# Kernel optimization log

Measured on AMD Instinct MI355X. Metric: run time of the kernel, lower is better.

Reference implementation:

```python
import jax, jax.numpy as jnp
import numpy as np

B, T, E = 2, 2048, 2048
H, HKV, DH = 16, 8, 128
G = H // HKV
WINDOW = 512
ROPE_THETA = 10000.0
EPS = 1e-6


def _rms_norm(x, w):
    # Gemma3RMSNorm: fp32 rms_norm with weight = 1 + w
    xf = x.astype(jnp.float32)
    y = xf * jax.lax.rsqrt(jnp.mean(xf * xf, axis=-1, keepdims=True) + EPS)
    return (y * (1.0 + w.astype(jnp.float32))).astype(x.dtype)


def _rotate_half(x):
    x1, x2 = x[..., : DH // 2], x[..., DH // 2 :]
    return jnp.concatenate((-x2, x1), axis=-1)


def setup_inputs() -> dict:
    key = jax.random.key(0)
    ks = jax.random.split(key, 5)
    s = 0.02
    return {
        "x": jax.random.normal(ks[0], (B, T, E), jnp.float32),
        "wq": jax.random.normal(ks[1], (H * DH, E), jnp.float32) * s,
        "wk": jax.random.normal(ks[2], (HKV * DH, E), jnp.float32) * s,
        "wv": jax.random.normal(ks[3], (HKV * DH, E), jnp.float32) * s,
        "wo": jax.random.normal(ks[4], (E, H * DH), jnp.float32) * s,
        "q_norm_w": jnp.zeros((DH,), jnp.float32),
        "k_norm_w": jnp.zeros((DH,), jnp.float32),
    }


def reference(x, wq, wk, wv, wo, q_norm_w, k_norm_w):
    # projections: [B,T,H,DH] -> [B,H,T,DH]
    q = (x @ wq.T).reshape(B, T, H, DH).transpose(0, 2, 1, 3)
    k = (x @ wk.T).reshape(B, T, HKV, DH).transpose(0, 2, 1, 3)
    v = (x @ wv.T).reshape(B, T, HKV, DH).transpose(0, 2, 1, 3)

    # QK-RMSNorm over head_dim
    q = _rms_norm(q, q_norm_w)
    k = _rms_norm(k, k_norm_w)

    # RoPE (prefill: positions 0..T-1)
    pos = jnp.arange(T, dtype=jnp.float32)
    inv_freq = 1.0 / (ROPE_THETA ** (jnp.arange(0, DH, 2, dtype=jnp.float32) / DH))
    freqs = pos[:, None] * inv_freq[None, :]          # [T, DH//2]
    emb = jnp.concatenate((freqs, freqs), axis=-1)    # [T, DH]
    cos = jnp.cos(emb)[None, None, :, :]
    sin = jnp.sin(emb)[None, None, :, :]
    q = q * cos + _rotate_half(q) * sin
    k = k * cos + _rotate_half(k) * sin

    # GQA attention with causal + sliding-window mask, fp32 scores
    q = q * (DH ** -0.5)
    qg = q.reshape(B, HKV, G, T, DH)
    att = jnp.einsum("bhgtd,bhkd->bhgtk", qg.astype(jnp.float32), k.astype(jnp.float32))

    dist = jnp.arange(T)[:, None] - jnp.arange(T)[None, :]   # [T, T]
    mask = (dist >= 0) & (dist <= WINDOW)
    att = jnp.where(mask[None, None, None, :, :], att, jnp.finfo(jnp.float32).min)
    att = jax.nn.softmax(att, axis=-1).astype(q.dtype)

    ctx = jnp.einsum("bhgtk,bhkd->bhgtd", att, v)
    out = ctx.reshape(B, H, T, DH).transpose(0, 2, 1, 3).reshape(B, T, H * DH)
    return out @ wo.T
```

## Files before the change

kernel.cpp:

```cpp
#include <hip/hip_runtime.h>
#include <hip/hip_bf16.h>
#include <stdint.h>

#define B_ 2
#define T_ 2048
#define E_ 2048
#define H_ 16
#define HKV_ 8
#define DH_ 128
#define WINDOW_ 512

typedef unsigned short ush;
typedef float f32x4 __attribute__((ext_vector_type(4)));
typedef __bf16 bf16x8 __attribute__((ext_vector_type(8)));
typedef uint32_t u32x4 __attribute__((ext_vector_type(4)));

static __device__ __forceinline__ ush f2bf(float f) {
    uint32_t u = __float_as_uint(f);
    uint32_t r = (u + 0x7fffu + ((u >> 16) & 1u)) >> 16;
    return (ush)r;
}
static __device__ __forceinline__ float bf2f(ush h) {
    return __uint_as_float(((uint32_t)h) << 16);
}

__global__ __launch_bounds__(256) void cast_kernel(const float* __restrict__ in,
                                                   ush* __restrict__ out, int n4) {
    int i = blockIdx.x * blockDim.x + threadIdx.x;
    if (i >= n4) return;
    float4 f = reinterpret_cast<const float4*>(in)[i];
    ushort4 o;
    o.x = f2bf(f.x); o.y = f2bf(f.y); o.z = f2bf(f.z); o.w = f2bf(f.w);
    reinterpret_cast<ushort4*>(out)[i] = o;
}

template <int MODE>
__global__ __launch_bounds__(256, 2) void gemm_bt(
    const ush* __restrict__ A, const ush* __restrict__ Bm,
    float* __restrict__ Cf, ush* __restrict__ q, ush* __restrict__ k, ush* __restrict__ vT,
    int M, int N, int K)
{
    __shared__ ush As[128 * 64];
    __shared__ ush Bs[128 * 64];
    const int tid = threadIdx.x;
    const int lane = tid & 63;
    const int wid = tid >> 6;
    const int wr = wid >> 1, wc = wid & 1;
    const int gm0 = blockIdx.x * 128, gn0 = blockIdx.y * 128;

    f32x4 acc[4][4] = {};

    const int l8 = lane >> 3;
    const int ce = (lane & 7) * 8;

    for (int kt = 0; kt < K; kt += 64) {
#pragma unroll
        for (int i = 0; i < 4; ++i) {
            const int rowbase = (i * 4 + wid) * 8;
            const int ra = rowbase + l8;
            const ush* ga = A + (size_t)(gm0 + ra) * K + kt + ce;
            __builtin_amdgcn_global_load_lds(
                (const __attribute__((address_space(1))) void*)ga,
                (__attribute__((address_space(3))) void*)(As + rowbase * 64), 16, 0, 0);
            const ush* gb = Bm + (size_t)(gn0 + ra) * K + kt + ce;
            __builtin_amdgcn_global_load_lds(
                (const __attribute__((address_space(1))) void*)gb,
                (__attribute__((address_space(3))) void*)(Bs + rowbase * 64), 16, 0, 0);
        }
        __syncthreads();

#pragma unroll
        for (int s = 0; s < 2; ++s) {
            bf16x8 aF[4], bF[4];
#pragma unroll
            for (int mm = 0; mm < 4; ++mm) {
                int r = wr * 64 + mm * 16 + (lane & 15);
                aF[mm] = *reinterpret_cast<const bf16x8*>(As + r * 64 + s * 32 + ((lane >> 4) * 8));
            }
#pragma unroll
            for (int nn = 0; nn < 4; ++nn) {
                int r = wc * 64 + nn * 16 + (lane & 15);
                bF[nn] = *reinterpret_cast<const bf16x8*>(Bs + r * 64 + s * 32 + ((lane >> 4) * 8));
            }
#pragma unroll
            for (int mm = 0; mm < 4; ++mm)
#pragma unroll
                for (int nn = 0; nn < 4; ++nn)
                    acc[mm][nn] = __builtin_amdgcn_mfma_f32_16x16x32_bf16(
                        aF[mm], bF[nn], acc[mm][nn], 0, 0, 0);
        }
        __syncthreads();
    }

    const int rsub = (lane >> 4) << 2;
    const int csub = lane & 15;
#pragma unroll
    for (int mm = 0; mm < 4; ++mm) {
        const int row0 = gm0 + wr * 64 + mm * 16 + rsub;
#pragma unroll
        for (int nn = 0; nn < 4; ++nn) {
            const int col = gn0 + wc * 64 + nn * 16 + csub;
#pragma unroll
            for (int r = 0; r < 4; ++r) {
                const int row = row0 + r;
                if (MODE == 1) {
                    Cf[(size_t)row * N + col] = acc[mm][nn][r];
                } else {
                    const int bb = row >> 11, tt = row & (T_ - 1);
                    const ush val = f2bf(acc[mm][nn][r]);
                    if (col < H_ * DH_) {
                        const int hh = col >> 7, d = col & 127;
                        q[((((size_t)bb * H_ + hh) * T_ + tt) << 7) + d] = val;
                    } else if (col < H_ * DH_ + HKV_ * DH_) {
                        const int c2 = col - H_ * DH_;
                        const int hh = c2 >> 7, d = c2 & 127;
                        k[((((size_t)bb * HKV_ + hh) * T_ + tt) << 7) + d] = val;
                    } else {
                        const int c2 = col - H_ * DH_ - HKV_ * DH_;
                        const int hh = c2 >> 7, d = c2 & 127;
                        vT[((size_t)((bb * HKV_ + hh) * DH_ + d) << 11) + tt] = val;
                    }
                }
            }
        }
    }
}

__global__ __launch_bounds__(256) void norm_rope(ush* __restrict__ q, ush* __restrict__ k,
                                                 const float* __restrict__ qw,
                                                 const float* __restrict__ kw)
{
    const int lane = threadIdx.x & 63;
    const int row = blockIdx.x * 4 + (threadIdx.x >> 6);
    const int NQ = B_ * H_ * T_;
    ush* p; const float* w; int t; bool isq = (row < NQ);
    if (isq) { p = q + ((size_t)row << 7); t = row & (T_ - 1); w = qw; }
    else     { int r2 = row - NQ; p = k + ((size_t)r2 << 7); t = r2 & (T_ - 1); w = kw; }

    float x0 = bf2f(p[lane]);
    float x1 = bf2f(p[lane + 64]);
    float ss = x0 * x0 + x1 * x1;
#pragma unroll
    for (int off = 32; off; off >>= 1) ss += __shfl_xor(ss, off);
    const float rms = rsqrtf(ss * (1.0f / 128.0f) + 1e-6f);
    float y0 = x0 * rms * (1.0f + w[lane]);
    float y1 = x1 * rms * (1.0f + w[lane + 64]);

    const float invf = expf(-(float)lane * 0.14391156831212787f);
    const float fr = (float)t * invf;
    const float c = cosf(fr), s = sinf(fr);
    float o0 = y0 * c - y1 * s;
    float o1 = y1 * c + y0 * s;
    if (isq) { o0 *= 0.08838834764831845f; o1 *= 0.08838834764831845f; }
    p[lane] = f2bf(o0);
    p[lane + 64] = f2bf(o1);
}

__global__ __launch_bounds__(256) void attn_mfma(const ush* __restrict__ q,
        const ush* __restrict__ k, const ush* __restrict__ vT, ush* __restrict__ ctx)
{
    __shared__ ush Ks[2][32 * 128];
    __shared__ ush Vs[2][128 * 32];
    const int tid = threadIdx.x;
    const int lane = tid & 63;
    const int w = tid >> 6;
    const int g = lane >> 4;
    const int t = lane & 15;

    int bi = blockIdx.x;
    bi = (bi & 7) * 128 + (bi >> 3);
    const int qtile = bi & 31;
    const int hh = (bi >> 5) & 15;
    const int b = bi >> 9;
    const int qb = qtile * 64;
    const int hkv = hh >> 1;

    const ush* qptr = q + ((((size_t)b * H_ + hh) * T_ + qb) << 7);
    const ush* kbase = k + (((size_t)b * HKV_ + hkv) << 18);
    const ush* vtbase = vT + (((size_t)b * HKV_ + hkv) << 18);

    bf16x8 qf[4];
#pragma unroll
    for (int c = 0; c < 4; ++c)
        qf[c] = *reinterpret_cast<const bf16x8*>(qptr + ((16 * w + t) << 7) + 32 * c + 8 * g);

    const int kstart = (qb >= WINDOW_) ? (qb - WINDOW_) : 0;
    const int nt = (qb + 64 - kstart) >> 5;

    auto stage = [&](int ti, int buf) {
        const int kt0 = kstart + (ti << 5);
#pragma unroll
        for (int i = 0; i < 2; ++i) {
            const int C = w * 128 + i * 64 + lane;
            {
                const int row = C >> 4, ch = C & 15;
                const ush* gk = kbase + ((size_t)(kt0 + row) << 7) + ch * 8;
                __builtin_amdgcn_global_load_lds(
                    (const __attribute__((address_space(1))) void*)gk,
                    (__attribute__((address_space(3))) void*)(&Ks[buf][(w * 128 + i * 64) * 8]),
                    16, 0, 0);
            }
            {
                const int row = C >> 2, ch = C & 3;
                const ush* gv = vtbase + ((size_t)row << 11) + kt0 + ch * 8;
                __builtin_amdgcn_global_load_lds(
                    (const __attribute__((address_space(1))) void*)gv,
                    (__attribute__((address_space(3))) void*)(&Vs[buf][(w * 128 + i * 64) * 8]),
                    16, 0, 0);
            }
        }
    };

    float m = -1e30f, lsum = 0.f;
    f32x4 o[8] = {};

    stage(0, 0);
    __syncthreads();

    for (int ti = 0; ti < nt; ++ti) {
        const int cur = ti & 1;
        if (ti + 1 < nt) stage(ti + 1, cur ^ 1);
        const int kt0 = kstart + (ti << 5);
        const int qw0 = qb + 16 * w;
        const bool active = (kt0 + 31 >= qw0 - WINDOW_) && (kt0 <= qw0 + 15);
        if (active) {
            f32x4 st[2] = {};
#pragma unroll
            for (int s = 0; s < 2; ++s)
#pragma unroll
                for (int c = 0; c < 4; ++c) {
                    bf16x8 kf = *reinterpret_cast<const bf16x8*>(
                        &Ks[cur][(16 * s + t) * 128 + 32 * c + 8 * g]);
                    st[s] = __builtin_amdgcn_mfma_f32_16x16x32_bf16(kf, qf[c], st[s], 0, 0, 0);
                }
            const int tg = qb + 16 * w + t;
            float e[2][4];
            float mymax = -3e38f;
#pragma unroll
            for (int s = 0; s < 2; ++s)
#pragma unroll
                for (int r = 0; r < 4; ++r) {
                    const int key = kt0 + 16 * s + 4 * g + r;
                    const int dist = tg - key;
                    const bool valid = (dist >= 0) && (dist <= WINDOW_);
                    const float sv = valid ? st[s][r] : -3e38f;
                    e[s][r] = sv;
                    mymax = fmaxf(mymax, sv);
                }
            mymax = fmaxf(mymax, __shfl_xor(mymax, 16));
            mymax = fmaxf(mymax, __shfl_xor(mymax, 32));
            const float mn = fmaxf(m, mymax);
            const float sc = __expf(m - mn);
            float esum = 0.f;
#pragma unroll
            for (int s = 0; s < 2; ++s)
#pragma unroll
                for (int r = 0; r < 4; ++r) {
                    const float ev = __expf(e[s][r] - mn);
                    e[s][r] = ev;
                    esum += ev;
                }
            esum += __shfl_xor(esum, 16);
            esum += __shfl_xor(esum, 32);
            lsum = lsum * sc + esum;
            m = mn;
#pragma unroll
            for (int ds = 0; ds < 8; ++ds) {
                o[ds][0] *= sc; o[ds][1] *= sc; o[ds][2] *= sc; o[ds][3] *= sc;
            }
            uint32_t word[2][2];
#pragma unroll
            for (int s = 0; s < 2; ++s)
#pragma unroll
                for (int wd = 0; wd < 2; ++wd)
                    word[s][wd] = (uint32_t)f2bf(e[s][2 * wd])
                                | ((uint32_t)f2bf(e[s][2 * wd + 1]) << 16);
            u32x4 bw;
#pragma unroll
            for (int e2 = 0; e2 < 4; ++e2) {
                const int srcl = 16 * (2 * (g & 1) + (e2 >> 1)) + t;
                const uint32_t v0 = __shfl(word[0][e2 & 1], srcl);
                const uint32_t v1 = __shfl(word[1][e2 & 1], srcl);
                bw[e2] = (g >= 2) ? v1 : v0;
            }
            const bf16x8 pF = __builtin_bit_cast(bf16x8, bw);
#pragma unroll
            for (int ds = 0; ds < 8; ++ds) {
                bf16x8 vtF = *reinterpret_cast<const bf16x8*>(
                    &Vs[cur][(16 * ds + t) * 32 + 8 * g]);
                o[ds] = __builtin_amdgcn_mfma_f32_16x16x32_bf16(vtF, pF, o[ds], 0, 0, 0);
            }
        }
        __syncthreads();
    }

    const float linv = 1.0f / lsum;
    ush* cptr = ctx + (((size_t)b * T_ + qb + 16 * w + t) * (H_ * DH_)) + hh * DH_;
#pragma unroll
    for (int ds = 0; ds < 8; ++ds) {
        ushort4 pk;
        pk.x = f2bf(o[ds][0] * linv);
        pk.y = f2bf(o[ds][1] * linv);
        pk.z = f2bf(o[ds][2] * linv);
        pk.w = f2bf(o[ds][3] * linv);
        *reinterpret_cast<ushort4*>(cptr + 16 * ds + 4 * g) = pk;
    }
}

extern "C" void kernel_launch(void* const* d_in, const int* in_sizes, int n_in,
                              void* d_out, int out_size, void* d_ws, size_t ws_size,
                              hipStream_t stream)
{
    const float* x   = (const float*)d_in[0];
    const float* wq  = (const float*)d_in[1];
    const float* wk  = (const float*)d_in[2];
    const float* wv  = (const float*)d_in[3];
    const float* wo  = (const float*)d_in[4];
    const float* qnw = (const float*)d_in[5];
    const float* knw = (const float*)d_in[6];
    float* out = (float*)d_out;

    ush* ws    = (ush*)d_ws;
    ush* xbf   = ws;
    ush* wqkv  = xbf  + 8388608;
    ush* wobf  = wqkv + 8388608;
    ush* qraw  = wobf + 4194304;
    ush* kraw  = qraw + 8388608;
    ush* vTb   = kraw + 4194304;
    ush* ctx   = vTb  + 4194304;

    cast_kernel<<<8192, 256, 0, stream>>>(x,  xbf, 2097152);
    cast_kernel<<<4096, 256, 0, stream>>>(wq, wqkv, 1048576);
    cast_kernel<<<2048, 256, 0, stream>>>(wk, wqkv + 4194304, 524288);
    cast_kernel<<<2048, 256, 0, stream>>>(wv, wqkv + 6291456, 524288);
    cast_kernel<<<4096, 256, 0, stream>>>(wo, wobf, 1048576);

    gemm_bt<0><<<dim3(32, 32), 256, 0, stream>>>(xbf, wqkv, nullptr, qraw, kraw, vTb,
                                                 4096, 4096, 2048);
    norm_rope<<<(65536 + 32768) / 4, 256, 0, stream>>>(qraw, kraw, qnw, knw);
    attn_mfma<<<1024, 256, 0, stream>>>(qraw, kraw, vTb, ctx);
    gemm_bt<1><<<dim3(32, 16), 256, 0, stream>>>(ctx, wobf, out, nullptr, nullptr, nullptr,
                                                 4096, 2048, 2048);
    (void)in_sizes; (void)n_in; (void)out_size; (void)ws_size;
}
```

Before: 260.4 us.

## Rewrite GEMM with 128x256 tiles, triple-buffered LDS pipeline and XOR swizzle

Replaces the 128x128 single-buffered GEMM with a 512-thread 128x256-tile kernel that prefetches two k-tiles ahead into a three-slot LDS ring, interleaving async global-to-LDS loads with MFMA work. LDS addresses are XOR-swizzled to avoid bank conflicts, and setprio raises priority around MFMA bursts. The intent is to hide global load latency and cut per-k-step barriers. The cost is much higher LDS use (144KB), which limits occupancy to one block per CU, and fewer blocks in the grid.

```diff
diff --git a/kernel.cpp b/kernel.cpp
--- a/kernel.cpp
+++ b/kernel.cpp
@@ -35,79 +35,132 @@
 }
 
 template <int MODE>
-__global__ __launch_bounds__(256, 2) void gemm_bt(
+__global__ __launch_bounds__(512, 2) void gemm_bt2(
     const ush* __restrict__ A, const ush* __restrict__ Bm,
     float* __restrict__ Cf, ush* __restrict__ q, ush* __restrict__ k, ush* __restrict__ vT,
     int M, int N, int K)
 {
-    __shared__ ush As[128 * 64];
-    __shared__ ush Bs[128 * 64];
+    __shared__ ush As[3][128 * 64];
+    __shared__ ush Bs[3][256 * 64];
     const int tid = threadIdx.x;
     const int lane = tid & 63;
     const int wid = tid >> 6;
-    const int wr = wid >> 1, wc = wid & 1;
-    const int gm0 = blockIdx.x * 128, gn0 = blockIdx.y * 128;
+    const int wr = wid >> 2, wc = wid & 3;
+    const int g = lane >> 4, t = lane & 15;
+    const int gm0 = blockIdx.x * 128, gn0 = blockIdx.y * 256;
 
     f32x4 acc[4][4] = {};
 
-    const int l8 = lane >> 3;
-    const int ce = (lane & 7) * 8;
-
-    for (int kt = 0; kt < K; kt += 64) {
-#pragma unroll
-        for (int i = 0; i < 4; ++i) {
-            const int rowbase = (i * 4 + wid) * 8;
-            const int ra = rowbase + l8;
-            const ush* ga = A + (size_t)(gm0 + ra) * K + kt + ce;
+    auto stageA2 = [&](int kt, int m3) {
+#pragma unroll
+        for (int i = 0; i < 2; ++i) {
+            const int C = i * 512 + tid;
+            const int r = C >> 3, c = C & 7;
+            const ush* src = A + (size_t)(gm0 + r) * K + (kt << 6) + ((c ^ (r & 7)) << 3);
             __builtin_amdgcn_global_load_lds(
-                (const __attribute__((address_space(1))) void*)ga,
-                (__attribute__((address_space(3))) void*)(As + rowbase * 64), 16, 0, 0);
-            const ush* gb = Bm + (size_t)(gn0 + ra) * K + kt + ce;
+                (const __attribute__((address_space(1))) void*)src,
+                (__attribute__((address_space(3))) void*)(&As[m3][C << 3]), 16, 0, 0);
+        }
+    };
+    auto stageB = [&](int kt, int m3, int i0, int i1) {
+        for (int i = i0; i < i1; ++i) {
+            const int C = i * 512 + tid;
+            const int r = C >> 3, c = C & 7;
+            const ush* src = Bm + (size_t)(gn0 + r) * K + (kt << 6) + ((c ^ (r & 7)) << 3);
             __builtin_amdgcn_global_load_lds(
-                (const __attribute__((address_space(1))) void*)gb,
-                (__attribute__((address_space(3))) void*)(Bs + rowbase * 64), 16, 0, 0);
-        }
-        __syncthreads();
-
-#pragma unroll
-        for (int s = 0; s < 2; ++s) {
-            bf16x8 aF[4], bF[4];
-#pragma unroll
-            for (int mm = 0; mm < 4; ++mm) {
-                int r = wr * 64 + mm * 16 + (lane & 15);
-                aF[mm] = *reinterpret_cast<const bf16x8*>(As + r * 64 + s * 32 + ((lane >> 4) * 8));
-            }
-#pragma unroll
-            for (int nn = 0; nn < 4; ++nn) {
-                int r = wc * 64 + nn * 16 + (lane & 15);
-                bF[nn] = *reinterpret_cast<const bf16x8*>(Bs + r * 64 + s * 32 + ((lane >> 4) * 8));
-            }
-#pragma unroll
-            for (int mm = 0; mm < 4; ++mm)
-#pragma unroll
-                for (int nn = 0; nn < 4; ++nn)
-                    acc[mm][nn] = __builtin_amdgcn_mfma_f32_16x16x32_bf16(
-                        aF[mm], bF[nn], acc[mm][nn], 0, 0, 0);
-        }
-        __syncthreads();
+                (const __attribute__((address_space(1))) void*)src,
+                (__attribute__((address_space(3))) void*)(&Bs[m3][C << 3]), 16, 0, 0);
+        }
+    };
+
+    const int nt = K >> 6;
+
+    stageA2(0, 0); stageB(0, 0, 0, 4);
+    stageA2(1, 1); stageB(1, 1, 0, 4);
+    asm volatile("s_waitcnt vmcnt(6)" ::: "memory");
+    __builtin_amdgcn_s_barrier();
+    __builtin_amdgcn_sched_barrier(0);
+
+    int m3 = 0;
+    for (int kt = 0; kt < nt; ++kt) {
+        const int st3 = (m3 + 2 >= 3) ? m3 - 1 : m3 + 2;
+        bf16x8 af[4][2], bfr[2][2];
+
+#pragma unroll
+        for (int mf = 0; mf < 4; ++mf)
+#pragma unroll
+            for (int ks = 0; ks < 2; ++ks) {
+                const int row = wr * 64 + mf * 16 + t;
+                af[mf][ks] = *reinterpret_cast<const bf16x8*>(
+                    &As[m3][row * 64 + ((((ks << 2) + g) ^ (t & 7)) << 3)]);
+            }
+#pragma unroll
+        for (int n2 = 0; n2 < 2; ++n2)
+#pragma unroll
+            for (int ks = 0; ks < 2; ++ks) {
+                const int row = wc * 64 + n2 * 16 + t;
+                bfr[n2][ks] = *reinterpret_cast<const bf16x8*>(
+                    &Bs[m3][row * 64 + ((((ks << 2) + g) ^ (t & 7)) << 3)]);
+            }
+        if (kt + 2 < nt) { stageA2(kt + 2, st3); stageB(kt + 2, st3, 0, 1); }
+        __builtin_amdgcn_s_setprio(1);
+#pragma unroll
+        for (int mf = 0; mf < 4; ++mf)
+#pragma unroll
+            for (int n2 = 0; n2 < 2; ++n2)
+#pragma unroll
+                for (int ks = 0; ks < 2; ++ks)
+                    acc[mf][n2] = __builtin_amdgcn_mfma_f32_16x16x32_bf16(
+                        af[mf][ks], bfr[n2][ks], acc[mf][n2], 0, 0, 0);
+        __builtin_amdgcn_s_setprio(0);
+        __builtin_amdgcn_s_barrier();
+        __builtin_amdgcn_sched_barrier(0);
+
+#pragma unroll
+        for (int n2 = 0; n2 < 2; ++n2)
+#pragma unroll
+            for (int ks = 0; ks < 2; ++ks) {
+                const int row = wc * 64 + (2 + n2) * 16 + t;
+                bfr[n2][ks] = *reinterpret_cast<const bf16x8*>(
+                    &Bs[m3][row * 64 + ((((ks << 2) + g) ^ (t & 7)) << 3)]);
+            }
+        if (kt + 2 < nt) stageB(kt + 2, st3, 1, 4);
+        __builtin_amdgcn_s_setprio(1);
+#pragma unroll
+        for (int mf = 0; mf < 4; ++mf)
+#pragma unroll
+            for (int n2 = 0; n2 < 2; ++n2)
+#pragma unroll
+                for (int ks = 0; ks < 2; ++ks)
+                    acc[mf][2 + n2] = __builtin_amdgcn_mfma_f32_16x16x32_bf16(
+                        af[mf][ks], bfr[n2][ks], acc[mf][2 + n2], 0, 0, 0);
+        __builtin_amdgcn_s_setprio(0);
+        if (kt + 1 < nt) {
+            if (kt + 2 < nt) asm volatile("s_waitcnt vmcnt(6)" ::: "memory");
+            else             asm volatile("s_waitcnt vmcnt(0)" ::: "memory");
+        }
+        __builtin_amdgcn_s_barrier();
+        __builtin_amdgcn_sched_barrier(0);
+
+        m3 = (m3 + 1 >= 3) ? 0 : m3 + 1;
     }
 
     const int rsub = (lane >> 4) << 2;
     const int csub = lane & 15;
 #pragma unroll
-    for (int mm = 0; mm < 4; ++mm) {
-        const int row0 = gm0 + wr * 64 + mm * 16 + rsub;
-#pragma unroll
-        for (int nn = 0; nn < 4; ++nn) {
-            const int col = gn0 + wc * 64 + nn * 16 + csub;
+    for (int mf = 0; mf < 4; ++mf) {
+        const int row0 = gm0 + wr * 64 + mf * 16 + rsub;
+#pragma unroll
+        for (int nf = 0; nf < 4; ++nf) {
+            const int col = gn0 + wc * 64 + nf * 16 + csub;
 #pragma unroll
             for (int r = 0; r < 4; ++r) {
                 const int row = row0 + r;
                 if (MODE == 1) {
-                    Cf[(size_t)row * N + col] = acc[mm][nn][r];
+                    Cf[(size_t)row * N + col] = acc[mf][nf][r];
                 } else {
                     const int bb = row >> 11, tt = row & (T_ - 1);
-                    const ush val = f2bf(acc[mm][nn][r]);
+                    const ush val = f2bf(acc[mf][nf][r]);
                     if (col < H_ * DH_) {
                         const int hh = col >> 7, d = col & 127;
                         q[((((size_t)bb * H_ + hh) * T_ + tt) << 7) + d] = val;
@@ -335,11 +388,11 @@
     cast_kernel<<<2048, 256, 0, stream>>>(wv, wqkv + 6291456, 524288);
     cast_kernel<<<4096, 256, 0, stream>>>(wo, wobf, 1048576);
 
-    gemm_bt<0><<<dim3(32, 32), 256, 0, stream>>>(xbf, wqkv, nullptr, qraw, kraw, vTb,
-                                                 4096, 4096, 2048);
+    gemm_bt2<0><<<dim3(32, 16), 512, 0, stream>>>(xbf, wqkv, nullptr, qraw, kraw, vTb,
+                                                  4096, 4096, 2048);
     norm_rope<<<(65536 + 32768) / 4, 256, 0, stream>>>(qraw, kraw, qnw, knw);
     attn_mfma<<<1024, 256, 0, stream>>>(qraw, kraw, vTb, ctx);
-    gemm_bt<1><<<dim3(32, 16), 256, 0, stream>>>(ctx, wobf, out, nullptr, nullptr, nullptr,
+    gemm_bt2<1><<<dim3(32, 8), 512, 0, stream>>>(ctx, wobf, out, nullptr, nullptr, nullptr,
                                                  4096, 2048, 2048);
     (void)in_sizes; (void)n_in; (void)out_size; (void)ws_size;
 }
```

Result: faster. 232.7 us (-10.7%).
